# Optimization experiments

Hardware: AMD Instinct MI355X
Metric: run time of the kernel (lower is better)

Reference implementation:

```python
import jax, jax.numpy as jnp
import numpy as np

# config constants (from init_kwargs)
MAX_WORD_LENGTH = 8
RESIDUAL_THRESHOLD = 1e-3
DECAY_FACTOR = 0.9


def setup_inputs() -> dict:
    key = jax.random.key(0)
    k1, k2 = jax.random.split(key)
    targets = jax.random.normal(k1, (8192, 1024), dtype=jnp.float32)
    codebook = jax.random.normal(k2, (4096, 1024), dtype=jnp.float32)
    return {"targets": targets, "codebook": codebook}


def reference(targets, codebook):
    """Batched greedy residual pursuit.

    targets:  [B, D] semantic vectors
    codebook: [K, D] syllable vectors
    Returns (indices [B, L] int32 with -1 where the per-sample loop broke,
             final residual [B, D]).
    """
    B = targets.shape[0]

    def step(carry, s):
        residual, active = carry  # [B, D], [B] bool
        # break condition checked BEFORE selecting, as in the torch loop
        norm = jnp.sqrt(jnp.sum(residual * residual, axis=-1))  # [B]
        active = active & (norm >= RESIDUAL_THRESHOLD)
        scores = jnp.einsum("bd,kd->bk", residual, codebook)  # [B, K]
        idx = jnp.argmax(scores, axis=-1)  # [B]
        decay = jnp.power(jnp.float32(DECAY_FACTOR), s.astype(jnp.float32))
        contribution = decay * codebook[idx]  # [B, D]
        residual = jnp.where(active[:, None], residual - contribution, residual)
        out_idx = jnp.where(active, idx, -1).astype(jnp.int32)
        return (residual, active), out_idx

    init = (targets, jnp.ones((B,), dtype=bool))
    (residual, _), idx_seq = jax.lax.scan(step, init, jnp.arange(MAX_WORD_LENGTH))
    indices = jnp.transpose(idx_seq)  # [B, L]
    return indices, residual
```

## Files before the change

### kernel.cpp

```cpp
#include <hip/hip_runtime.h>
#include <hip/hip_bf16.h>
#include <math.h>

#define NB 8192
#define NK 4096
#define ND 1024
#define NL 8
#define RES_THR 1e-3f

typedef __bf16 bf16x8 __attribute__((ext_vector_type(8)));
typedef float f32x4 __attribute__((ext_vector_type(4)));

#define MFMA16(a, b, c) __builtin_amdgcn_mfma_f32_16x16x32_bf16(a, b, c, 0, 0, 0)

#define GLOAD(g, l)                                                        \
  __builtin_amdgcn_global_load_lds(                                        \
      (const __attribute__((address_space(1))) void*)(g),                  \
      (__attribute__((address_space(3))) void*)(l), 16, 0, 0)

__device__ __forceinline__ unsigned short f2bf(float x) {
  __hip_bfloat16 h = __float2bfloat16(x);
  return __builtin_bit_cast(unsigned short, h);
}
__device__ __forceinline__ float bf2f(unsigned short u) {
  return __bfloat162float(__builtin_bit_cast(__hip_bfloat16, u));
}

__device__ __forceinline__ float wave_reduce_sum(float v) {
#pragma unroll
  for (int off = 32; off > 0; off >>= 1) v += __shfl_down(v, off);
  return v;
}

__device__ __forceinline__ void top2_merge(float& v1, int& k1, float& v2,
                                           int& k2, float w1, int j1, float w2,
                                           int j2) {
  if (w1 > v1 || (w1 == v1 && j1 < k1)) {
    if (v1 > w2 || (v1 == w2 && k1 < j2)) { v2 = v1; k2 = k1; }
    else { v2 = w2; k2 = j2; }
    v1 = w1; k1 = j1;
  } else {
    if (w1 > v2 || (w1 == v2 && j1 < k2)) { v2 = w1; k2 = j1; }
  }
}

__global__ __launch_bounds__(256) void k_prep(const float* __restrict__ cb,
                                              unsigned short* __restrict__ Bh) {
  int b = blockIdx.x, t = threadIdx.x;
  float4 v = ((const float4*)(cb + (size_t)b * ND))[t];
  ushort4 h;
  h.x = f2bf(v.x); h.y = f2bf(v.y); h.z = f2bf(v.z); h.w = f2bf(v.w);
  ((ushort4*)(Bh + (size_t)b * ND))[t] = h;
}

__global__ __launch_bounds__(256) void k_init(const float* __restrict__ tgt,
                                              float* __restrict__ resid,
                                              unsigned short* __restrict__ Ah,
                                              int* __restrict__ active) {
  int b = blockIdx.x, t = threadIdx.x;
  float4 v = ((const float4*)(tgt + (size_t)b * ND))[t];
  ((float4*)(resid + (size_t)b * ND))[t] = v;
  ushort4 h;
  h.x = f2bf(v.x); h.y = f2bf(v.y); h.z = f2bf(v.z); h.w = f2bf(v.w);
  ((ushort4*)(Ah + (size_t)b * ND))[t] = h;
  float ss = v.x * v.x + v.y * v.y + v.z * v.z + v.w * v.w;
  ss = wave_reduce_sum(ss);
  __shared__ float red[4];
  if ((t & 63) == 0) red[t >> 6] = ss;
  __syncthreads();
  if (t == 0) {
    float tot = red[0] + red[1] + red[2] + red[3];
    active[b] = (sqrtf(tot) >= RES_THR) ? 1 : 0;
  }
}

__global__ __launch_bounds__(512) void k_score0(
    const unsigned short* __restrict__ Ah, const unsigned short* __restrict__ Bh,
    float4* __restrict__ part, unsigned short* __restrict__ sc) {
  __shared__ __align__(16) char sA0[32768];
  __shared__ __align__(16) char sA1[32768];
  __shared__ __align__(16) char sB0[32768];
  __shared__ __align__(16) char sB1[32768];
  const int tid = threadIdx.x;
  const int lane = tid & 63;
  const int swzid = (blockIdx.x & 7) * 64 + (blockIdx.x >> 3);
  const int bm = swzid >> 4;
  const int bn = swzid & 15;
  const int wid = tid >> 6;
  const int wr = wid >> 2;
  const int wc = wid & 3;

  const int srow = tid >> 3;
  const int sblk = (tid & 7) ^ (srow & 7);
  const unsigned short* aSrc = Ah + (size_t)(bm * 256 + srow) * ND + sblk * 8;
  const unsigned short* bSrc = Bh + (size_t)(bn * 256 + srow) * ND + sblk * 8;

  const int lr = lane & 15;
  const int lk = lane >> 4;
  const int swz = lr & 7;
  const int kb0 = ((lk ^ swz) << 4);
  const int kb1 = (((4 + lk) ^ swz) << 4);

  f32x4 acc[8][4];
#pragma unroll
  for (int m = 0; m < 8; ++m)
#pragma unroll
    for (int n = 0; n < 4; ++n) acc[m][n] = (f32x4)(0.f);

#pragma unroll
  for (int rr = 0; rr < 4; ++rr) {
    GLOAD(aSrc + (size_t)(rr * 64) * ND, sA0 + rr * 8192 + tid * 16);
    GLOAD(bSrc + (size_t)(rr * 64) * ND, sB0 + rr * 8192 + tid * 16);
  }
#pragma unroll
  for (int rr = 0; rr < 4; ++rr) {
    GLOAD(aSrc + (size_t)(rr * 64) * ND + 64, sA1 + rr * 8192 + tid * 16);
    GLOAD(bSrc + (size_t)(rr * 64) * ND + 64, sB1 + rr * 8192 + tid * 16);
  }

#pragma unroll 1
  for (int kt = 0; kt < 16; ++kt) {
    const char* pa = (kt & 1) ? sA1 : sA0;
    const char* pb = (kt & 1) ? sB1 : sB0;
    if (kt < 15) {
      asm volatile("s_waitcnt vmcnt(8)" ::: "memory");
    } else {
      asm volatile("s_waitcnt vmcnt(0)" ::: "memory");
    }
    __builtin_amdgcn_s_barrier();
    bf16x8 af0[8], bf0[4];
#pragma unroll
    for (int m = 0; m < 8; ++m)
      af0[m] = *(const bf16x8*)(pa + (wr * 128 + m * 16 + lr) * 128 + kb0);
#pragma unroll
    for (int n = 0; n < 4; ++n)
      bf0[n] = *(const bf16x8*)(pb + (wc * 64 + n * 16 + lr) * 128 + kb0);
    __builtin_amdgcn_s_setprio(1);
#pragma unroll
    for (int m = 0; m < 8; ++m)
#pragma unroll
      for (int n = 0; n < 4; ++n) acc[m][n] = MFMA16(af0[m], bf0[n], acc[m][n]);
    __builtin_amdgcn_s_setprio(0);
    bf16x8 af1[8], bf1[4];
#pragma unroll
    for (int m = 0; m < 8; ++m)
      af1[m] = *(const bf16x8*)(pa + (wr * 128 + m * 16 + lr) * 128 + kb1);
#pragma unroll
    for (int n = 0; n < 4; ++n)
      bf1[n] = *(const bf16x8*)(pb + (wc * 64 + n * 16 + lr) * 128 + kb1);
    __syncthreads();
    if (kt < 14) {
      const int k0 = (kt + 2) << 6;
      char* da = (kt & 1) ? sA1 : sA0;
      char* db = (kt & 1) ? sB1 : sB0;
#pragma unroll
      for (int rr = 0; rr < 4; ++rr) {
        GLOAD(aSrc + (size_t)(rr * 64) * ND + k0, da + rr * 8192 + tid * 16);
        GLOAD(bSrc + (size_t)(rr * 64) * ND + k0, db + rr * 8192 + tid * 16);
      }
    }
    __builtin_amdgcn_s_setprio(1);
#pragma unroll
    for (int m = 0; m < 8; ++m)
#pragma unroll
      for (int n = 0; n < 4; ++n) acc[m][n] = MFMA16(af1[m], bf1[n], acc[m][n]);
    __builtin_amdgcn_s_setprio(0);
  }
  __syncthreads();

  if (sc) {
#pragma unroll
    for (int m = 0; m < 8; ++m) {
      int row = bm * 256 + wr * 128 + m * 16 + lk * 4;
#pragma unroll
      for (int q = 0; q < 4; ++q)
#pragma unroll
        for (int n = 0; n < 4; ++n)
          sc[(size_t)(row + q) * NK + bn * 256 + wc * 64 + n * 16 + lr] =
              f2bf(acc[m][n][q]);
    }
  }

  if (part) {
    float4* red = (float4*)sA0;
#pragma unroll
    for (int m = 0; m < 8; ++m) {
#pragma unroll
      for (int q = 0; q < 4; ++q) {
        float v1 = acc[m][0][q];
        int k1 = bn * 256 + wc * 64 + lr;
        float v2 = -INFINITY;
        int k2 = 0x7fffffff;
#pragma unroll
        for (int n = 1; n < 4; ++n) {
          top2_merge(v1, k1, v2, k2, acc[m][n][q],
                     bn * 256 + wc * 64 + n * 16 + lr, -INFINITY, 0x7fffffff);
        }
#pragma unroll
        for (int msk = 1; msk < 16; msk <<= 1) {
          float ov1 = __shfl_xor(v1, msk);
          int ok1 = __shfl_xor(k1, msk);
          float ov2 = __shfl_xor(v2, msk);
          int ok2 = __shfl_xor(k2, msk);
          top2_merge(v1, k1, v2, k2, ov1, ok1, ov2, ok2);
        }
        if (lr == 0) {
          int row = wr * 128 + m * 16 + lk * 4 + q;
          red[row * 4 + wc] =
              make_float4(v1, __int_as_float(k1), v2, __int_as_float(k2));
        }
      }
    }
    __syncthreads();
    if (tid < 256) {
      float4 e0 = red[tid * 4 + 0];
      float v1 = e0.x; int k1 = __float_as_int(e0.y);
      float v2 = e0.z; int k2 = __float_as_int(e0.w);
#pragma unroll
      for (int j = 1; j < 4; ++j) {
        float4 e = red[tid * 4 + j];
        top2_merge(v1, k1, v2, k2, e.x, __float_as_int(e.y), e.z,
                   __float_as_int(e.w));
      }
      part[(size_t)(bm * 256 + tid) * 16 + bn] =
          make_float4(v1, __int_as_float(k1), v2, __int_as_float(k2));
    }
  }
}

__global__ __launch_bounds__(512) void k_gram(const unsigned short* __restrict__ Bh,
                                              unsigned short* __restrict__ G) {
  __shared__ __align__(16) char sA0[32768];
  __shared__ __align__(16) char sA1[32768];
  __shared__ __align__(16) char sB0[32768];
  __shared__ __align__(16) char sB1[32768];
  const int tid = threadIdx.x;
  const int lane = tid & 63;
  const int bm = blockIdx.x >> 4;
  const int bn = blockIdx.x & 15;
  const int wid = tid >> 6;
  const int wr = wid >> 2;
  const int wc = wid & 3;
  const int srow = tid >> 3;
  const int sblk = (tid & 7) ^ (srow & 7);
  const unsigned short* aSrc = Bh + (size_t)(bm * 256 + srow) * ND + sblk * 8;
  const unsigned short* bSrc = Bh + (size_t)(bn * 256 + srow) * ND + sblk * 8;
  const int lr = lane & 15;
  const int lk = lane >> 4;
  const int swz = lr & 7;
  const int kb0 = ((lk ^ swz) << 4);
  const int kb1 = (((4 + lk) ^ swz) << 4);

  f32x4 acc[8][4];
#pragma unroll
  for (int m = 0; m < 8; ++m)
#pragma unroll
    for (int n = 0; n < 4; ++n) acc[m][n] = (f32x4)(0.f);

#pragma unroll
  for (int rr = 0; rr < 4; ++rr) {
    GLOAD(aSrc + (size_t)(rr * 64) * ND, sA0 + rr * 8192 + tid * 16);
    GLOAD(bSrc + (size_t)(rr * 64) * ND, sB0 + rr * 8192 + tid * 16);
  }
#pragma unroll
  for (int rr = 0; rr < 4; ++rr) {
    GLOAD(aSrc + (size_t)(rr * 64) * ND + 64, sA1 + rr * 8192 + tid * 16);
    GLOAD(bSrc + (size_t)(rr * 64) * ND + 64, sB1 + rr * 8192 + tid * 16);
  }
#pragma unroll 1
  for (int kt = 0; kt < 16; ++kt) {
    const char* pa = (kt & 1) ? sA1 : sA0;
    const char* pb = (kt & 1) ? sB1 : sB0;
    if (kt < 15) {
      asm volatile("s_waitcnt vmcnt(8)" ::: "memory");
    } else {
      asm volatile("s_waitcnt vmcnt(0)" ::: "memory");
    }
    __builtin_amdgcn_s_barrier();
    bf16x8 af0[8], bf0[4];
#pragma unroll
    for (int m = 0; m < 8; ++m)
      af0[m] = *(const bf16x8*)(pa + (wr * 128 + m * 16 + lr) * 128 + kb0);
#pragma unroll
    for (int n = 0; n < 4; ++n)
      bf0[n] = *(const bf16x8*)(pb + (wc * 64 + n * 16 + lr) * 128 + kb0);
    __builtin_amdgcn_s_setprio(1);
#pragma unroll
    for (int m = 0; m < 8; ++m)
#pragma unroll
      for (int n = 0; n < 4; ++n) acc[m][n] = MFMA16(af0[m], bf0[n], acc[m][n]);
    __builtin_amdgcn_s_setprio(0);
    bf16x8 af1[8], bf1[4];
#pragma unroll
    for (int m = 0; m < 8; ++m)
      af1[m] = *(const bf16x8*)(pa + (wr * 128 + m * 16 + lr) * 128 + kb1);
#pragma unroll
    for (int n = 0; n < 4; ++n)
      bf1[n] = *(const bf16x8*)(pb + (wc * 64 + n * 16 + lr) * 128 + kb1);
    __syncthreads();
    if (kt < 14) {
      const int k0 = (kt + 2) << 6;
      char* da = (kt & 1) ? sA1 : sA0;
      char* db = (kt & 1) ? sB1 : sB0;
#pragma unroll
      for (int rr = 0; rr < 4; ++rr) {
        GLOAD(aSrc + (size_t)(rr * 64) * ND + k0, da + rr * 8192 + tid * 16);
        GLOAD(bSrc + (size_t)(rr * 64) * ND + k0, db + rr * 8192 + tid * 16);
      }
    }
    __builtin_amdgcn_s_setprio(1);
#pragma unroll
    for (int m = 0; m < 8; ++m)
#pragma unroll
      for (int n = 0; n < 4; ++n) acc[m][n] = MFMA16(af1[m], bf1[n], acc[m][n]);
    __builtin_amdgcn_s_setprio(0);
  }
#pragma unroll
  for (int m = 0; m < 8; ++m) {
    int row = bm * 256 + wr * 128 + m * 16 + lk * 4;
#pragma unroll
    for (int q = 0; q < 4; ++q)
#pragma unroll
      for (int n = 0; n < 4; ++n)
        G[(size_t)(row + q) * NK + bn * 256 + wc * 64 + n * 16 + lr] =
            f2bf(acc[m][n][q]);
  }
}

__global__ __launch_bounds__(256) void k_all(
    const unsigned short* __restrict__ sc0, const unsigned short* __restrict__ G,
    const float* __restrict__ cb, float* __restrict__ resid,
    float* __restrict__ out_idx, const int* __restrict__ active0) {
  const int b = blockIdx.x, t = threadIdx.x;
  __shared__ float s_max[4];
  __shared__ float s_nrm[4];
  __shared__ float s_red[4];
  __shared__ int s_cnt;
  __shared__ int s_k[64];
  __shared__ float s_bv;
  __shared__ int s_bk;

  float4 r = ((const float4*)(resid + (size_t)b * ND))[t];

  float scv[16];
  {
    const unsigned short* srow = sc0 + (size_t)b * NK;
    uint4 v0 = *(const uint4*)(srow + t * 8);
    uint4 v1 = *(const uint4*)(srow + 2048 + t * 8);
    unsigned w[8] = {v0.x, v0.y, v0.z, v0.w, v1.x, v1.y, v1.z, v1.w};
#pragma unroll
    for (int j = 0; j < 8; ++j) {
      scv[2 * j] = bf2f((unsigned short)(w[j] & 0xffff));
      scv[2 * j + 1] = bf2f((unsigned short)(w[j] >> 16));
    }
  }
  int act = active0[b];
  float decay = 1.0f;

#pragma unroll 1
  for (int s = 0; s < NL; ++s) {
    float m = scv[0];
#pragma unroll
    for (int i = 1; i < 16; ++i) m = fmaxf(m, scv[i]);
    float ss = r.x * r.x + r.y * r.y + r.z * r.z + r.w * r.w;
#pragma unroll
    for (int off = 32; off > 0; off >>= 1) {
      m = fmaxf(m, __shfl_xor(m, off));
      ss += __shfl_xor(ss, off);
    }
    if ((t & 63) == 0) { s_max[t >> 6] = m; s_nrm[t >> 6] = ss; }
    if (t == 0) { s_cnt = 0; s_bv = -INFINITY; s_bk = 0x7fffffff; }
    __syncthreads();
    const float M = fmaxf(fmaxf(s_max[0], s_max[1]), fmaxf(s_max[2], s_max[3]));
    const float nrm = s_nrm[0] + s_nrm[1] + s_nrm[2] + s_nrm[3];
    act = (act && sqrtf(nrm) >= RES_THR) ? 1 : 0;
    const float margin = (s == 0) ? 2.5f : 6.0f;
#pragma unroll
    for (int i = 0; i < 16; ++i) {
      if (scv[i] >= M - margin) {
        int col = (i < 8) ? (t * 8 + i) : (2048 + t * 8 + (i - 8));
        int pos = atomicAdd(&s_cnt, 1);
        if (pos < 64) s_k[pos] = col;
      }
    }
    __syncthreads();
    int cnt = s_cnt < 64 ? s_cnt : 64;
    for (int c = 0; c < cnt; ++c) {
      int k = s_k[c];
      float4 cv = ((const float4*)(cb + (size_t)k * ND))[t];
      float dd = r.x * cv.x + r.y * cv.y + r.z * cv.z + r.w * cv.w;
      dd = wave_reduce_sum(dd);
      if ((t & 63) == 0) s_red[t >> 6] = dd;
      __syncthreads();
      if (t == 0) {
        float scr = s_red[0] + s_red[1] + s_red[2] + s_red[3];
        if (scr > s_bv || (scr == s_bv && k < s_bk)) { s_bv = scr; s_bk = k; }
      }
      __syncthreads();
    }
    int kbest = s_bk;
    if (t == 0) out_idx[(size_t)b * NL + s] = act ? (float)kbest : -1.0f;
    if (act) {
      float4 cv = ((const float4*)(cb + (size_t)kbest * ND))[t];
      r.x -= decay * cv.x;
      r.y -= decay * cv.y;
      r.z -= decay * cv.z;
      r.w -= decay * cv.w;
      if (s < NL - 1) {
        const unsigned short* grow = G + (size_t)kbest * NK;
        uint4 g0 = *(const uint4*)(grow + t * 8);
        uint4 g1 = *(const uint4*)(grow + 2048 + t * 8);
        unsigned w[8] = {g0.x, g0.y, g0.z, g0.w, g1.x, g1.y, g1.z, g1.w};
#pragma unroll
        for (int j = 0; j < 8; ++j) {
          scv[2 * j] -= decay * bf2f((unsigned short)(w[j] & 0xffff));
          scv[2 * j + 1] -= decay * bf2f((unsigned short)(w[j] >> 16));
        }
      }
    }
    decay *= 0.9f;
    __syncthreads();
  }
  ((float4*)(resid + (size_t)b * ND))[t] = r;
}

__global__ __launch_bounds__(256) void k_update(
    float* __restrict__ resid, const float* __restrict__ cb,
    const float4* __restrict__ part, int* __restrict__ active,
    float* __restrict__ out_idx, unsigned short* __restrict__ Ah, float decay,
    int s, int nseg, float margin) {
  int b = blockIdx.x, t = threadIdx.x;
  __shared__ int s_cnt;
  __shared__ int s_k[32];
  __shared__ float s_red[4];
  __shared__ float s_bv;
  __shared__ int s_bk;

  float4 r = ((const float4*)(resid + (size_t)b * ND))[t];

  if (t < 2 * nseg) {
    float4 e = part[(size_t)b * 16 + (t >> 1)];
    float v = (t & 1) ? e.z : e.x;
    int k = __float_as_int((t & 1) ? e.w : e.y);
    float M = v;
    for (int off = nseg; off > 0; off >>= 1) M = fmaxf(M, __shfl_xor(M, off));
    bool cand = (v >= M - margin);
    unsigned long long mask = __ballot(cand);
    int slot = __popcll(mask & ((1ull << t) - 1ull));
    if (cand && slot < 32) s_k[slot] = k;
    if (t == 0) {
      int n = (int)__popcll(mask);
      s_cnt = n < 32 ? n : 32;
      s_bv = -INFINITY;
      s_bk = 0x7fffffff;
    }
  }
  __syncthreads();
  int cnt = s_cnt;
  for (int c = 0; c < cnt; ++c) {
    int k = s_k[c];
    float4 cv = ((const float4*)(cb + (size_t)k * ND))[t];
    float dd = r.x * cv.x + r.y * cv.y + r.z * cv.z + r.w * cv.w;
    dd = wave_reduce_sum(dd);
    if ((t & 63) == 0) s_red[t >> 6] = dd;
    __syncthreads();
    if (t == 0) {
      float sc = s_red[0] + s_red[1] + s_red[2] + s_red[3];
      if (sc > s_bv || (sc == s_bv && k < s_bk)) { s_bv = sc; s_bk = k; }
    }
    __syncthreads();
  }
  int kbest = s_bk;
  int act = active[b];
  float4 cv = ((const float4*)(cb + (size_t)kbest * ND))[t];
  if (act) {
    r.x -= decay * cv.x;
    r.y -= decay * cv.y;
    r.z -= decay * cv.z;
    r.w -= decay * cv.w;
  }
  ((float4*)(resid + (size_t)b * ND))[t] = r;
  if (Ah) {
    ushort4 h;
    h.x = f2bf(r.x); h.y = f2bf(r.y); h.z = f2bf(r.z); h.w = f2bf(r.w);
    ((ushort4*)(Ah + (size_t)b * ND))[t] = h;
  }
  float ss = r.x * r.x + r.y * r.y + r.z * r.z + r.w * r.w;
  ss = wave_reduce_sum(ss);
  if ((t & 63) == 0) s_red[t >> 6] = ss;
  __syncthreads();
  if (t == 0) {
    float tot = s_red[0] + s_red[1] + s_red[2] + s_red[3];
    out_idx[(size_t)b * NL + s] = act ? (float)kbest : -1.0f;
    active[b] = (act && sqrtf(tot) >= RES_THR) ? 1 : 0;
  }
}

extern "C" void kernel_launch(void* const* d_in, const int* in_sizes, int n_in,
                              void* d_out, int out_size, void* d_ws,
                              size_t ws_size, hipStream_t stream) {
  const float* targets = (const float*)d_in[0];
  const float* codebook = (const float*)d_in[1];
  float* out = (float*)d_out;
  float* out_idx = out;
  float* resid = out + (size_t)NB * NL;

  char* ws = (char*)d_ws;
  const size_t SC_SZ = (size_t)NB * NK * 2;
  const size_t G_SZ = (size_t)NK * NK * 2;
  const size_t AH_SZ = (size_t)NB * ND * 2;
  const size_t BH_SZ = (size_t)NK * ND * 2;
  const size_t PART_SZ = (size_t)NB * 16 * 16;
  const size_t NEED = SC_SZ + G_SZ + AH_SZ + BH_SZ + PART_SZ + 32768;

  if (ws_size >= NEED) {
    unsigned short* scores = (unsigned short*)ws;
    unsigned short* G = (unsigned short*)(ws + SC_SZ);
    unsigned short* Ah = (unsigned short*)(ws + SC_SZ + G_SZ);
    unsigned short* Bh = (unsigned short*)(ws + SC_SZ + G_SZ + AH_SZ);
    int* active = (int*)(ws + SC_SZ + G_SZ + AH_SZ + BH_SZ + PART_SZ);

    k_prep<<<NK, 256, 0, stream>>>(codebook, Bh);
    k_init<<<NB, 256, 0, stream>>>(targets, resid, Ah, active);
    k_gram<<<256, 512, 0, stream>>>(Bh, G);
    k_score0<<<(NB / 256) * (NK / 256), 512, 0, stream>>>(Ah, Bh, nullptr,
                                                          scores);
    k_all<<<NB, 256, 0, stream>>>(scores, G, codebook, resid, out_idx, active);
  } else {
    float4* part = (float4*)ws;
    int* active = (int*)(ws + PART_SZ);
    unsigned short* Ah = (unsigned short*)(ws + PART_SZ + 65536);
    unsigned short* Bh = Ah + (size_t)NB * ND;

    k_prep<<<NK, 256, 0, stream>>>(codebook, Bh);
    k_init<<<NB, 256, 0, stream>>>(targets, resid, Ah, active);
    for (int s = 0; s < NL; ++s) {
      k_score0<<<(NB / 256) * (NK / 256), 512, 0, stream>>>(Ah, Bh, part,
                                                            nullptr);
      float ds = (float)pow(0.9, (double)s);
      k_update<<<NB, 256, 0, stream>>>(resid, codebook, part, active, out_idx,
                                       Ah, ds, s, 16, 2.5f);
    }
  }
}
```

Before: 288.0 us.

## Process one sample per wavefront in k_all to drop block barriers

Restructures the greedy pursuit kernel so each 64-lane wavefront owns a whole sample instead of a 256-thread block per sample. Each lane now holds 64 scores and 16 residual elements, and all reductions become wave shuffles. This removes the __syncthreads barriers and shared-memory reductions from the candidate rescoring loop. It also skips rescoring when only one candidate passes the margin. The cost is much higher register pressure (64 score floats plus 16 residual floats per lane), which may lower occupancy, and less memory-level parallelism per sample.

Result: no change. 283.6 us (-1.5%).

```diff
diff --git a/kernel.cpp b/kernel.cpp
--- a/kernel.cpp
+++ b/kernel.cpp
@@ -331,29 +331,29 @@
     const unsigned short* __restrict__ sc0, const unsigned short* __restrict__ G,
     const float* __restrict__ cb, float* __restrict__ resid,
     float* __restrict__ out_idx, const int* __restrict__ active0) {
-  const int b = blockIdx.x, t = threadIdx.x;
-  __shared__ float s_max[4];
-  __shared__ float s_nrm[4];
-  __shared__ float s_red[4];
-  __shared__ int s_cnt;
-  __shared__ int s_k[64];
-  __shared__ float s_bv;
-  __shared__ int s_bk;
-
-  float4 r = ((const float4*)(resid + (size_t)b * ND))[t];
-
-  float scv[16];
+  const int wv = threadIdx.x >> 6;
+  const int lane = threadIdx.x & 63;
+  const int b = blockIdx.x * 4 + wv;
+  __shared__ int ls_cnt[4];
+  __shared__ int ls_k[4][32];
+
+  float scv[64];
   {
-    const unsigned short* srow = sc0 + (size_t)b * NK;
-    uint4 v0 = *(const uint4*)(srow + t * 8);
-    uint4 v1 = *(const uint4*)(srow + 2048 + t * 8);
-    unsigned w[8] = {v0.x, v0.y, v0.z, v0.w, v1.x, v1.y, v1.z, v1.w};
+    const unsigned short* srow = sc0 + (size_t)b * NK + lane * 64;
 #pragma unroll
     for (int j = 0; j < 8; ++j) {
-      scv[2 * j] = bf2f((unsigned short)(w[j] & 0xffff));
-      scv[2 * j + 1] = bf2f((unsigned short)(w[j] >> 16));
-    }
-  }
+      uint4 v = *(const uint4*)(srow + j * 8);
+      unsigned w[4] = {v.x, v.y, v.z, v.w};
+#pragma unroll
+      for (int q = 0; q < 4; ++q) {
+        scv[j * 8 + 2 * q] = bf2f((unsigned short)(w[q] & 0xffff));
+        scv[j * 8 + 2 * q + 1] = bf2f((unsigned short)(w[q] >> 16));
+      }
+    }
+  }
+  const float4* rbase = (const float4*)(resid + (size_t)b * ND + lane * 16);
+  float4 r0 = rbase[0], r1 = rbase[1], r2 = rbase[2], r3 = rbase[3];
+
   int act = active0[b];
   float decay = 1.0f;
 
@@ -361,67 +361,87 @@
   for (int s = 0; s < NL; ++s) {
     float m = scv[0];
 #pragma unroll
-    for (int i = 1; i < 16; ++i) m = fmaxf(m, scv[i]);
-    float ss = r.x * r.x + r.y * r.y + r.z * r.z + r.w * r.w;
+    for (int i = 1; i < 64; ++i) m = fmaxf(m, scv[i]);
+    float ss = r0.x * r0.x + r0.y * r0.y + r0.z * r0.z + r0.w * r0.w +
+               r1.x * r1.x + r1.y * r1.y + r1.z * r1.z + r1.w * r1.w +
+               r2.x * r2.x + r2.y * r2.y + r2.z * r2.z + r2.w * r2.w +
+               r3.x * r3.x + r3.y * r3.y + r3.z * r3.z + r3.w * r3.w;
 #pragma unroll
     for (int off = 32; off > 0; off >>= 1) {
       m = fmaxf(m, __shfl_xor(m, off));
       ss += __shfl_xor(ss, off);
     }
-    if ((t & 63) == 0) { s_max[t >> 6] = m; s_nrm[t >> 6] = ss; }
-    if (t == 0) { s_cnt = 0; s_bv = -INFINITY; s_bk = 0x7fffffff; }
-    __syncthreads();
-    const float M = fmaxf(fmaxf(s_max[0], s_max[1]), fmaxf(s_max[2], s_max[3]));
-    const float nrm = s_nrm[0] + s_nrm[1] + s_nrm[2] + s_nrm[3];
-    act = (act && sqrtf(nrm) >= RES_THR) ? 1 : 0;
-    const float margin = (s == 0) ? 2.5f : 6.0f;
-#pragma unroll
-    for (int i = 0; i < 16; ++i) {
-      if (scv[i] >= M - margin) {
-        int col = (i < 8) ? (t * 8 + i) : (2048 + t * 8 + (i - 8));
-        int pos = atomicAdd(&s_cnt, 1);
-        if (pos < 64) s_k[pos] = col;
-      }
-    }
-    __syncthreads();
-    int cnt = s_cnt < 64 ? s_cnt : 64;
-    for (int c = 0; c < cnt; ++c) {
-      int k = s_k[c];
-      float4 cv = ((const float4*)(cb + (size_t)k * ND))[t];
-      float dd = r.x * cv.x + r.y * cv.y + r.z * cv.z + r.w * cv.w;
-      dd = wave_reduce_sum(dd);
-      if ((t & 63) == 0) s_red[t >> 6] = dd;
-      __syncthreads();
-      if (t == 0) {
-        float scr = s_red[0] + s_red[1] + s_red[2] + s_red[3];
-        if (scr > s_bv || (scr == s_bv && k < s_bk)) { s_bv = scr; s_bk = k; }
-      }
-      __syncthreads();
-    }
-    int kbest = s_bk;
-    if (t == 0) out_idx[(size_t)b * NL + s] = act ? (float)kbest : -1.0f;
+    act = (act && sqrtf(ss) >= RES_THR) ? 1 : 0;
+    const float thr = m - ((s == 0) ? 2.5f : 6.0f);
+    if (lane == 0) ls_cnt[wv] = 0;
+    asm volatile("s_waitcnt lgkmcnt(0)" ::: "memory");
+#pragma unroll
+    for (int i = 0; i < 64; ++i) {
+      if (scv[i] >= thr) {
+        int pos = atomicAdd(&ls_cnt[wv], 1);
+        if (pos < 32) ls_k[wv][pos] = lane * 64 + i;
+      }
+    }
+    asm volatile("s_waitcnt lgkmcnt(0)" ::: "memory");
+    int cnt = ls_cnt[wv];
+    cnt = cnt < 32 ? cnt : 32;
+    int kbest;
+    if (cnt <= 1) {
+      kbest = ls_k[wv][0];
+    } else {
+      float bv = -INFINITY;
+      int bk = 0x7fffffff;
+      for (int c = 0; c < cnt; ++c) {
+        int k = ls_k[wv][c];
+        const float4* cbr = (const float4*)(cb + (size_t)k * ND + lane * 16);
+        float4 c0 = cbr[0], c1 = cbr[1], c2 = cbr[2], c3 = cbr[3];
+        float dd = r0.x * c0.x + r0.y * c0.y + r0.z * c0.z + r0.w * c0.w +
+                   r1.x * c1.x + r1.y * c1.y + r1.z * c1.z + r1.w * c1.w +
+                   r2.x * c2.x + r2.y * c2.y + r2.z * c2.z + r2.w * c2.w +
+                   r3.x * c3.x + r3.y * c3.y + r3.z * c3.z + r3.w * c3.w;
+#pragma unroll
+        for (int off = 32; off > 0; off >>= 1) dd += __shfl_xor(dd, off);
+        if (dd > bv || (dd == bv && k < bk)) { bv = dd; bk = k; }
+      }
+      kbest = bk;
+    }
+    if (lane == 0) out_idx[(size_t)b * NL + s] = act ? (float)kbest : -1.0f;
     if (act) {
-      float4 cv = ((const float4*)(cb + (size_t)kbest * ND))[t];
-      r.x -= decay * cv.x;
-      r.y -= decay * cv.y;
-      r.z -= decay * cv.z;
-      r.w -= decay * cv.w;
+      const float4* cbr = (const float4*)(cb + (size_t)kbest * ND + lane * 16);
+      float4 c0 = cbr[0], c1 = cbr[1], c2 = cbr[2], c3 = cbr[3];
+      r0.x -= decay * c0.x; r0.y -= decay * c0.y;
+      r0.z -= decay * c0.z; r0.w -= decay * c0.w;
+      r1.x -= decay * c1.x; r1.y -= decay * c1.y;
+      r1.z -= decay * c1.z; r1.w -= decay * c1.w;
+      r2.x -= decay * c2.x; r2.y -= decay * c2.y;
+      r2.z -= decay * c2.z; r2.w -= decay * c2.w;
+      r3.x -= decay * c3.x; r3.y -= decay * c3.y;
+      r3.z -= decay * c3.z; r3.w -= decay * c3.w;
       if (s < NL - 1) {
-        const unsigned short* grow = G + (size_t)kbest * NK;
-        uint4 g0 = *(const uint4*)(grow + t * 8);
-        uint4 g1 = *(const uint4*)(grow + 2048 + t * 8);
-        unsigned w[8] = {g0.x, g0.y, g0.z, g0.w, g1.x, g1.y, g1.z, g1.w};
-#pragma unroll
-        for (int j = 0; j < 8; ++j) {
+        const unsigned short* grow = G + (size_t)kbest * NK + lane * 64;
+        uint4 g0 = *(const uint4*)(grow + 0);
+        uint4 g1 = *(const uint4*)(grow + 8);
+        uint4 g2 = *(const uint4*)(grow + 16);
+        uint4 g3 = *(const uint4*)(grow + 24);
+        uint4 g4 = *(const uint4*)(grow + 32);
+        uint4 g5 = *(const uint4*)(grow + 40);
+        uint4 g6 = *(const uint4*)(grow + 48);
+        uint4 g7 = *(const uint4*)(grow + 56);
+        unsigned w[32] = {g0.x, g0.y, g0.z, g0.w, g1.x, g1.y, g1.z, g1.w,
+                          g2.x, g2.y, g2.z, g2.w, g3.x, g3.y, g3.z, g3.w,
+                          g4.x, g4.y, g4.z, g4.w, g5.x, g5.y, g5.z, g5.w,
+                          g6.x, g6.y, g6.z, g6.w, g7.x, g7.y, g7.z, g7.w};
+#pragma unroll
+        for (int j = 0; j < 32; ++j) {
           scv[2 * j] -= decay * bf2f((unsigned short)(w[j] & 0xffff));
           scv[2 * j + 1] -= decay * bf2f((unsigned short)(w[j] >> 16));
         }
       }
     }
     decay *= 0.9f;
-    __syncthreads();
-  }
-  ((float4*)(resid + (size_t)b * ND))[t] = r;
+  }
+  float4* rw = (float4*)(resid + (size_t)b * ND + lane * 16);
+  rw[0] = r0; rw[1] = r1; rw[2] = r2; rw[3] = r3;
 }
 
 __global__ __launch_bounds__(256) void k_update(
@@ -525,7 +545,8 @@
     k_gram<<<256, 512, 0, stream>>>(Bh, G);
     k_score0<<<(NB / 256) * (NK / 256), 512, 0, stream>>>(Ah, Bh, nullptr,
                                                           scores);
-    k_all<<<NB, 256, 0, stream>>>(scores, G, codebook, resid, out_idx, active);
+    k_all<<<NB / 4, 256, 0, stream>>>(scores, G, codebook, resid, out_idx,
+                                      active);
   } else {
     float4* part = (float4*)ws;
     int* active = (int*)(ws + PART_SZ);
```
